# Optimization experiments

Hardware: AMD Instinct MI355X
Metric: run time of the kernel (lower is better)

Reference implementation:

```python
import jax, jax.numpy as jnp
import numpy as np
from jax import lax

B, S, K, D = 256, 256, 64, 128


def setup_inputs() -> dict:
    key = jax.random.key(0)
    k0, k1, k2, k3, k4, k5 = jax.random.split(key, 6)
    encoded_sents = jax.random.normal(k0, (B, S, D), dtype=jnp.float32)
    mask = jax.random.randint(k1, (B, S), 0, 2) > 0  # bool sentence-availability mask
    keys = jax.random.normal(k2, (B, K, D), dtype=jnp.float32) * 0.1
    U = jax.random.normal(k3, (D, D), dtype=jnp.float32) * 0.05
    V = jax.random.normal(k4, (D, D), dtype=jnp.float32) * 0.05
    W = jax.random.normal(k5, (D, D), dtype=jnp.float32) * 0.05
    return {"encoded_sents": encoded_sents, "mask": mask, "keys": keys,
            "U": U, "V": V, "W": W}


def reference(encoded_sents, mask, keys, U, V, W):
    """Recurrent entity network (return_last=True).

    encoded_sents: [B, S, D]; mask: [B, S] bool; keys: [B, K, D]; U/V/W: [D, D].
    Original TF code gathers active batch rows per step, runs EntityCell, and
    scatters the delta back; mathematically equivalent to a masked update over
    the full batch, expressed here as a lax.scan over time.
    """
    def step(h, xm):
        s, m = xm                      # s: [B, D], m: [B] bool
        # gate g_i = sigmoid(s . (h_i + k_i))  -> [B, K]
        g = jax.nn.sigmoid(jnp.einsum('bd,bkd->bk', s, h + keys))
        # h_tilde = act(hU + kV + sW)  -> [B, K, D]
        h_tilde = jax.nn.relu(
            jnp.einsum('bkd,de->bke', h, U)
            + jnp.einsum('bkd,de->bke', keys, V)
            + jnp.einsum('bd,de->be', s, W)[:, None, :]
        )
        upd = h + g[..., None] * h_tilde
        # tf.nn.l2_normalize along last axis
        upd = upd / jnp.sqrt(jnp.maximum(jnp.sum(upd * upd, axis=-1, keepdims=True), 1e-12))
        # scatter-back semantics: only active rows change
        h_new = jnp.where(m[:, None, None], upd, h)
        return h_new, None

    h0 = jnp.zeros_like(keys)  # get_initial_state() tiled over batch
    h_final, _ = lax.scan(step, h0, (encoded_sents.transpose(1, 0, 2), mask.T))
    return h_final  # [B, K, D]
```

## Files before the change

kernel.cpp:

```cpp
#include <hip/hip_runtime.h>
#include <math.h>

#define BB 256
#define SS 256
#define KK 64
#define DD 128

typedef short bf16x8 __attribute__((ext_vector_type(8)));
typedef float f32x4 __attribute__((ext_vector_type(4)));

__device__ __forceinline__ unsigned short bf16_rne(float x) {
  unsigned u = __float_as_uint(x);
  unsigned r = ((u >> 16) & 1u) + 0x7fffu;
  return (unsigned short)((u + r) >> 16);
}

__global__ __launch_bounds__(256) void kv_kernel(const float* __restrict__ keys,
                                                 const float* __restrict__ V,
                                                 float* __restrict__ kV)
{
    __shared__ __align__(16) float Ks[KK][DD];
    __shared__ __align__(16) float Vs[DD][DD];
    const int b = blockIdx.x;
    const int t = threadIdx.x;
    const float* kb = keys + (size_t)b * KK * DD;
    for (int i = t; i < KK * DD / 4; i += 256) ((float4*)Ks)[i] = ((const float4*)kb)[i];
    for (int i = t; i < DD * DD / 4; i += 256) ((float4*)Vs)[i] = ((const float4*)V)[i];
    __syncthreads();

    const int e0 = (t & 15) * 8;
    const int k0 = (t >> 4) * 4;
    float acc[4][8];
#pragma unroll
    for (int i = 0; i < 4; ++i)
#pragma unroll
        for (int j = 0; j < 8; ++j) acc[i][j] = 0.f;

#pragma unroll 4
    for (int d = 0; d < DD; ++d) {
        float aa[4] = {Ks[k0 + 0][d], Ks[k0 + 1][d], Ks[k0 + 2][d], Ks[k0 + 3][d]};
        float4 v0 = *(const float4*)&Vs[d][e0];
        float4 v1 = *(const float4*)&Vs[d][e0 + 4];
        float vv[8] = {v0.x, v0.y, v0.z, v0.w, v1.x, v1.y, v1.z, v1.w};
#pragma unroll
        for (int i = 0; i < 4; ++i)
#pragma unroll
            for (int j = 0; j < 8; ++j) acc[i][j] = fmaf(aa[i], vv[j], acc[i][j]);
    }
    float* o = kV + (size_t)b * KK * DD;
#pragma unroll
    for (int i = 0; i < 4; ++i)
#pragma unroll
        for (int j = 0; j < 8; j += 4) {
            float4 w4 = {acc[i][j], acc[i][j + 1], acc[i][j + 2], acc[i][j + 3]};
            *(float4*)&o[(k0 + i) * DD + e0 + j] = w4;
        }
}

__global__ __launch_bounds__(256) void sw_kernel(const float* __restrict__ enc,
                                                 const float* __restrict__ W,
                                                 float* __restrict__ sW)
{
    __shared__ __align__(16) float Es[64][DD];
    __shared__ __align__(16) float Ws[DD][DD];
    const int blk = blockIdx.x;
    const int b = blk >> 2;
    const int tt = blk & 3;
    const int t = threadIdx.x;
    const float* eb = enc + ((size_t)b * SS + tt * 64) * DD;
    for (int i = t; i < 64 * DD / 4; i += 256) ((float4*)Es)[i] = ((const float4*)eb)[i];
    for (int i = t; i < DD * DD / 4; i += 256) ((float4*)Ws)[i] = ((const float4*)W)[i];
    __syncthreads();

    const int e0 = (t & 15) * 8;
    const int r0 = (t >> 4) * 4;
    float acc[4][8];
#pragma unroll
    for (int i = 0; i < 4; ++i)
#pragma unroll
        for (int j = 0; j < 8; ++j) acc[i][j] = 0.f;

#pragma unroll 4
    for (int d = 0; d < DD; ++d) {
        float aa[4] = {Es[r0 + 0][d], Es[r0 + 1][d], Es[r0 + 2][d], Es[r0 + 3][d]};
        float4 v0 = *(const float4*)&Ws[d][e0];
        float4 v1 = *(const float4*)&Ws[d][e0 + 4];
        float vv[8] = {v0.x, v0.y, v0.z, v0.w, v1.x, v1.y, v1.z, v1.w};
#pragma unroll
        for (int i = 0; i < 4; ++i)
#pragma unroll
            for (int j = 0; j < 8; ++j) acc[i][j] = fmaf(aa[i], vv[j], acc[i][j]);
    }
    float* o = sW + ((size_t)b * SS + tt * 64) * DD;
#pragma unroll
    for (int i = 0; i < 4; ++i)
#pragma unroll
        for (int j = 0; j < 8; j += 4) {
            float4 w4 = {acc[i][j], acc[i][j + 1], acc[i][j + 2], acc[i][j + 3]};
            *(float4*)&o[(r0 + i) * DD + e0 + j] = w4;
        }
}

__global__ __launch_bounds__(256) void sk_kernel(const float* __restrict__ enc,
                                                 const float* __restrict__ keys,
                                                 float* __restrict__ sk)
{
    __shared__ __align__(16) float Es[64][DD];
    __shared__ __align__(16) float Ks[KK][DD];
    const int blk = blockIdx.x;
    const int b = blk >> 2;
    const int tt = blk & 3;
    const int t = threadIdx.x;
    const float* eb = enc + ((size_t)b * SS + tt * 64) * DD;
    const float* kb = keys + (size_t)b * KK * DD;
    for (int i = t; i < 64 * DD / 4; i += 256) ((float4*)Es)[i] = ((const float4*)eb)[i];
    for (int i = t; i < KK * DD / 4; i += 256) ((float4*)Ks)[i] = ((const float4*)kb)[i];
    __syncthreads();

    const int r0 = (t >> 4) * 4;
    const int k0 = (t & 15) * 4;
    float acc[4][4];
#pragma unroll
    for (int i = 0; i < 4; ++i)
#pragma unroll
        for (int j = 0; j < 4; ++j) acc[i][j] = 0.f;

#pragma unroll 4
    for (int d = 0; d < DD; ++d) {
        float er[4], kr[4];
#pragma unroll
        for (int i = 0; i < 4; ++i) er[i] = Es[r0 + i][d];
#pragma unroll
        for (int j = 0; j < 4; ++j) kr[j] = Ks[k0 + j][d];
#pragma unroll
        for (int i = 0; i < 4; ++i)
#pragma unroll
            for (int j = 0; j < 4; ++j) acc[i][j] = fmaf(er[i], kr[j], acc[i][j]);
    }
    float* o = sk + ((size_t)b * SS + tt * 64) * KK;
#pragma unroll
    for (int i = 0; i < 4; ++i) {
        float4 w4 = {acc[i][0], acc[i][1], acc[i][2], acc[i][3]};
        *(float4*)&o[(r0 + i) * KK + k0] = w4;
    }
}

__global__ void ufrag_kernel(const float* __restrict__ U,
                             unsigned short* __restrict__ Ufh,
                             unsigned short* __restrict__ Ufl)
{
    const int blk = blockIdx.x;
    const int ntg = blk >> 2, kt = blk & 3;
    const int l = threadIdx.x;
    const int e = ntg * 16 + (l & 15);
    const int d0 = kt * 32 + (l >> 4) * 8;
#pragma unroll
    for (int j = 0; j < 8; ++j) {
        float x = U[(d0 + j) * DD + e];
        unsigned short hi = bf16_rne(x);
        float rem = x - __uint_as_float(((unsigned)hi) << 16);
        unsigned short lo = bf16_rne(rem);
        int idx = (blk * 64 + l) * 8 + j;
        Ufh[idx] = hi;
        Ufl[idx] = lo;
    }
}

__global__ __launch_bounds__(512, 2) void entnet_main(
    const float* __restrict__ enc,
    const int*   __restrict__ mask,
    const float* __restrict__ sWg,
    const float* __restrict__ skg,
    const float* __restrict__ kVg,
    const unsigned short* __restrict__ Ufh,
    const unsigned short* __restrict__ Ufl,
    float*       __restrict__ out)
{
    __shared__ __align__(16) unsigned short hAhi[4][4][64][8];
    __shared__ __align__(16) unsigned short hAlo[4][4][64][8];
    __shared__ __align__(16) unsigned short shi_sh[2][DD];
    __shared__ __align__(16) unsigned short slo_sh[2][DD];
    __shared__ __align__(16) float sW_sh[2][DD];
    __shared__ __align__(16) float sk_sh[2][KK];
    __shared__ float g_sh[KK];
    __shared__ float rowsq_sh[2][KK];
    __shared__ int act_sh[SS];
    __shared__ int m_sh[SS];
    __shared__ int nact_sh;

    const int b = blockIdx.x;
    const int t = threadIdx.x;
    const int w = t >> 6, l = t & 63;
    const int mt = w & 3, eh = w >> 2;
    const int gi = l >> 4, li = l & 15;
    const int slot_r = l ^ ((l >> 2) & 3);
    const int role = t >> 7;

    if (t < SS) m_sh[t] = mask[b * SS + t];
    {
        unsigned int* p = (unsigned int*)&hAhi[0][0][0][0];
        unsigned int* q = (unsigned int*)&hAlo[0][0][0][0];
        for (int i = t; i < 4 * 4 * 64 * 8 / 2; i += 512) { p[i] = 0u; q[i] = 0u; }
    }
    __syncthreads();
    if (t == 0) {
        int c = 0;
        for (int i = 0; i < SS; ++i) if (m_sh[i]) act_sh[c++] = i;
        nact_sh = c;
    }

    bf16x8 ufh[4][4], ufl[4][4];
#pragma unroll
    for (int nt = 0; nt < 4; ++nt)
#pragma unroll
        for (int kt = 0; kt < 4; ++kt) {
            int ntg = eh * 4 + nt;
            int off = ((ntg * 4 + kt) * 64 + l) * 8;
            ufh[nt][kt] = *(const bf16x8*)&Ufh[off];
            ufl[nt][kt] = *(const bf16x8*)&Ufl[off];
        }
    float kvreg[4][4];
#pragma unroll
    for (int nt = 0; nt < 4; ++nt)
#pragma unroll
        for (int reg = 0; reg < 4; ++reg) {
            int k = 16 * mt + 4 * gi + reg;
            int e = 64 * eh + 16 * nt + li;
            kvreg[nt][reg] = kVg[((size_t)b * KK + k) * DD + e];
        }
    f32x4 hreg[4];
#pragma unroll
    for (int nt = 0; nt < 4; ++nt) hreg[nt] = (f32x4){0.f, 0.f, 0.f, 0.f};
    __syncthreads();

    const int nact = nact_sh;
    if (nact > 0 && t < 320) {
        int t0i = act_sh[0];
        if (role == 0) {
            float x = enc[((size_t)b * SS + t0i) * DD + t];
            unsigned u = __float_as_uint(x);
            shi_sh[0][t] = (unsigned short)(u >> 16);
            float rem = x - __uint_as_float(u & 0xffff0000u);
            slo_sh[0][t] = (unsigned short)(__float_as_uint(rem) >> 16);
        } else if (role == 1) {
            sW_sh[0][t - 128] = sWg[((size_t)b * SS + t0i) * DD + (t - 128)];
        } else {
            sk_sh[0][t - 256] = skg[((size_t)b * SS + t0i) * KK + (t - 256)];
        }
    }
    __syncthreads();

    for (int ai = 0; ai < nact; ++ai) {
        const int cur = ai & 1, nxt = cur ^ 1;
        float pf = 0.f;
        const bool have = (ai + 1 < nact);
        if (have && t < 320) {
            int tn = act_sh[ai + 1];
            if (role == 0)      pf = enc[((size_t)b * SS + tn) * DD + t];
            else if (role == 1) pf = sWg[((size_t)b * SS + tn) * DD + (t - 128)];
            else                pf = skg[((size_t)b * SS + tn) * KK + (t - 256)];
        }

        f32x4 acc[4];
#pragma unroll
        for (int nt = 0; nt < 4; ++nt) acc[nt] = (f32x4){0.f, 0.f, 0.f, 0.f};
        f32x4 gacc = (f32x4){0.f, 0.f, 0.f, 0.f};
#pragma unroll
        for (int kt = 0; kt < 4; ++kt) {
            bf16x8 ah = *(const bf16x8*)&hAhi[kt][mt][slot_r][0];
            bf16x8 al = *(const bf16x8*)&hAlo[kt][mt][slot_r][0];
#pragma unroll
            for (int nt = 0; nt < 4; ++nt) {
                acc[nt] = __builtin_amdgcn_mfma_f32_16x16x32_bf16(ah, ufh[nt][kt], acc[nt], 0, 0, 0);
                acc[nt] = __builtin_amdgcn_mfma_f32_16x16x32_bf16(al, ufh[nt][kt], acc[nt], 0, 0, 0);
                acc[nt] = __builtin_amdgcn_mfma_f32_16x16x32_bf16(ah, ufl[nt][kt], acc[nt], 0, 0, 0);
            }
            if (eh == 0) {
                bf16x8 sh = *(const bf16x8*)&shi_sh[cur][32 * kt + 8 * gi];
                bf16x8 sl = *(const bf16x8*)&slo_sh[cur][32 * kt + 8 * gi];
                gacc = __builtin_amdgcn_mfma_f32_16x16x32_bf16(ah, sh, gacc, 0, 0, 0);
                gacc = __builtin_amdgcn_mfma_f32_16x16x32_bf16(al, sh, gacc, 0, 0, 0);
                gacc = __builtin_amdgcn_mfma_f32_16x16x32_bf16(ah, sl, gacc, 0, 0, 0);
            }
        }
        if (eh == 0 && li == 0) {
#pragma unroll
            for (int reg = 0; reg < 4; ++reg) {
                int k = 16 * mt + 4 * gi + reg;
                float x = gacc[reg] + sk_sh[cur][k];
                g_sh[k] = 1.f / (1.f + __expf(-x));
            }
        }
        __syncthreads();

        float g4[4], sw4[4];
#pragma unroll
        for (int reg = 0; reg < 4; ++reg) g4[reg] = g_sh[16 * mt + 4 * gi + reg];
#pragma unroll
        for (int nt = 0; nt < 4; ++nt) sw4[nt] = sW_sh[cur][64 * eh + 16 * nt + li];
        f32x4 upd[4];
        float ss[4] = {0.f, 0.f, 0.f, 0.f};
#pragma unroll
        for (int nt = 0; nt < 4; ++nt)
#pragma unroll
            for (int reg = 0; reg < 4; ++reg) {
                float v = acc[nt][reg] + kvreg[nt][reg] + sw4[nt];
                v = fmaxf(v, 0.f);
                float u = fmaf(g4[reg], v, hreg[nt][reg]);
                upd[nt][reg] = u;
                ss[reg] = fmaf(u, u, ss[reg]);
            }
#pragma unroll
        for (int m = 1; m < 16; m <<= 1)
#pragma unroll
            for (int reg = 0; reg < 4; ++reg) ss[reg] += __shfl_xor(ss[reg], m);
        if (li == 0) {
#pragma unroll
            for (int reg = 0; reg < 4; ++reg)
                rowsq_sh[eh][16 * mt + 4 * gi + reg] = ss[reg];
        }
        __syncthreads();

        float rinv[4];
#pragma unroll
        for (int reg = 0; reg < 4; ++reg) {
            float tot = ss[reg] + rowsq_sh[1 - eh][16 * mt + 4 * gi + reg];
            rinv[reg] = rsqrtf(fmaxf(tot, 1e-12f));
        }
#pragma unroll
        for (int nt = 0; nt < 4; ++nt) {
            int kt_w = 2 * eh + (nt >> 1);
            int b23  = (2 * nt + (li >> 3)) & 3;
            int j    = l & 7;
#pragma unroll
            for (int reg = 0; reg < 4; ++reg) {
                float hn = upd[nt][reg] * rinv[reg];
                hreg[nt][reg] = hn;
                unsigned u = __float_as_uint(hn);
                unsigned short hi = (unsigned short)(u >> 16);
                float rem = hn - __uint_as_float(u & 0xffff0000u);
                unsigned short lo = (unsigned short)(__float_as_uint(rem) >> 16);
                int le = (4 * gi + reg) | (b23 << 4);
                int slot_w = le ^ ((le >> 2) & 3);
                hAhi[kt_w][mt][slot_w][j] = hi;
                hAlo[kt_w][mt][slot_w][j] = lo;
            }
        }
        if (have && t < 320) {
            if (role == 0) {
                unsigned u = __float_as_uint(pf);
                shi_sh[nxt][t] = (unsigned short)(u >> 16);
                float rem = pf - __uint_as_float(u & 0xffff0000u);
                slo_sh[nxt][t] = (unsigned short)(__float_as_uint(rem) >> 16);
            } else if (role == 1) sW_sh[nxt][t - 128] = pf;
            else                  sk_sh[nxt][t - 256] = pf;
        }
        __syncthreads();
    }

#pragma unroll
    for (int nt = 0; nt < 4; ++nt)
#pragma unroll
        for (int reg = 0; reg < 4; ++reg) {
            int k = 16 * mt + 4 * gi + reg;
            int e = 64 * eh + 16 * nt + li;
            out[((size_t)b * KK + k) * DD + e] = hreg[nt][reg];
        }
}

extern "C" void kernel_launch(void* const* d_in, const int* in_sizes, int n_in,
                              void* d_out, int out_size, void* d_ws, size_t ws_size,
                              hipStream_t stream)
{
    const float* enc  = (const float*)d_in[0];
    const int*   mask = (const int*)  d_in[1];
    const float* keys = (const float*)d_in[2];
    const float* U    = (const float*)d_in[3];
    const float* V    = (const float*)d_in[4];
    const float* W    = (const float*)d_in[5];
    float* out = (float*)d_out;

    float* sW = (float*)d_ws;
    float* sk = sW + (size_t)BB * SS * DD;
    float* kV = sk + (size_t)BB * SS * KK;
    unsigned short* Ufh = (unsigned short*)(kV + (size_t)BB * KK * DD);
    unsigned short* Ufl = Ufh + 8 * 4 * 64 * 8;

    kv_kernel<<<BB, 256, 0, stream>>>(keys, V, kV);
    sw_kernel<<<BB * 4, 256, 0, stream>>>(enc, W, sW);
    sk_kernel<<<BB * 4, 256, 0, stream>>>(enc, keys, sk);
    ufrag_kernel<<<32, 64, 0, stream>>>(U, Ufh, Ufl);
    entnet_main<<<BB, 512, 0, stream>>>(enc, mask, sW, sk, kV, Ufh, Ufl, out);
}
```

Baseline: 494.3 us.

## Split each batch row across four blocks by key rows and fuse sW/sk kernels

The main recurrent kernel is repartitioned so that each batch item's 64 key rows are divided among four 256-thread blocks, each owning 16 rows, instead of one 512-thread block per batch. This launches 1024 blocks rather than 256, which fills more compute units and shortens the per-step serial chain. The gate dot product is now split across the four waves and combined through shared memory. Block indices are remapped so the four blocks of a batch land on the same XCD, and the sW and sk precompute kernels are fused into one launch that reuses the loaded encoder tile. In exchange, every block redundantly loads the s/sW vectors and keeps its own copy of the U fragments.

New measurement: 648.0 us. 1.31x slower.

```diff
diff --git a/kernel.cpp b/kernel.cpp
--- a/kernel.cpp
+++ b/kernel.cpp
@@ -57,9 +57,11 @@
         }
 }
 
-__global__ __launch_bounds__(256) void sw_kernel(const float* __restrict__ enc,
-                                                 const float* __restrict__ W,
-                                                 float* __restrict__ sW)
+__global__ __launch_bounds__(256) void swsk_kernel(const float* __restrict__ enc,
+                                                   const float* __restrict__ W,
+                                                   const float* __restrict__ keys,
+                                                   float* __restrict__ sW,
+                                                   float* __restrict__ sk)
 {
     __shared__ __align__(16) float Es[64][DD];
     __shared__ __align__(16) float Ws[DD][DD];
@@ -72,76 +74,66 @@
     for (int i = t; i < DD * DD / 4; i += 256) ((float4*)Ws)[i] = ((const float4*)W)[i];
     __syncthreads();
 
-    const int e0 = (t & 15) * 8;
-    const int r0 = (t >> 4) * 4;
-    float acc[4][8];
-#pragma unroll
-    for (int i = 0; i < 4; ++i)
-#pragma unroll
-        for (int j = 0; j < 8; ++j) acc[i][j] = 0.f;
-
+    {
+        const int e0 = (t & 15) * 8;
+        const int r0 = (t >> 4) * 4;
+        float acc[4][8];
+#pragma unroll
+        for (int i = 0; i < 4; ++i)
+#pragma unroll
+            for (int j = 0; j < 8; ++j) acc[i][j] = 0.f;
 #pragma unroll 4
-    for (int d = 0; d < DD; ++d) {
-        float aa[4] = {Es[r0 + 0][d], Es[r0 + 1][d], Es[r0 + 2][d], Es[r0 + 3][d]};
-        float4 v0 = *(const float4*)&Ws[d][e0];
-        float4 v1 = *(const float4*)&Ws[d][e0 + 4];
-        float vv[8] = {v0.x, v0.y, v0.z, v0.w, v1.x, v1.y, v1.z, v1.w};
+        for (int d = 0; d < DD; ++d) {
+            float aa[4] = {Es[r0 + 0][d], Es[r0 + 1][d], Es[r0 + 2][d], Es[r0 + 3][d]};
+            float4 v0 = *(const float4*)&Ws[d][e0];
+            float4 v1 = *(const float4*)&Ws[d][e0 + 4];
+            float vv[8] = {v0.x, v0.y, v0.z, v0.w, v1.x, v1.y, v1.z, v1.w};
+#pragma unroll
+            for (int i = 0; i < 4; ++i)
+#pragma unroll
+                for (int j = 0; j < 8; ++j) acc[i][j] = fmaf(aa[i], vv[j], acc[i][j]);
+        }
+        float* o = sW + ((size_t)b * SS + tt * 64) * DD;
 #pragma unroll
         for (int i = 0; i < 4; ++i)
 #pragma unroll
-            for (int j = 0; j < 8; ++j) acc[i][j] = fmaf(aa[i], vv[j], acc[i][j]);
-    }
-    float* o = sW + ((size_t)b * SS + tt * 64) * DD;
-#pragma unroll
-    for (int i = 0; i < 4; ++i)
-#pragma unroll
-        for (int j = 0; j < 8; j += 4) {
-            float4 w4 = {acc[i][j], acc[i][j + 1], acc[i][j + 2], acc[i][j + 3]};
-            *(float4*)&o[(r0 + i) * DD + e0 + j] = w4;
-        }
-}
-
-__global__ __launch_bounds__(256) void sk_kernel(const float* __restrict__ enc,
-                                                 const float* __restrict__ keys,
-                                                 float* __restrict__ sk)
-{
-    __shared__ __align__(16) float Es[64][DD];
-    __shared__ __align__(16) float Ks[KK][DD];
-    const int blk = blockIdx.x;
-    const int b = blk >> 2;
-    const int tt = blk & 3;
-    const int t = threadIdx.x;
-    const float* eb = enc + ((size_t)b * SS + tt * 64) * DD;
-    const float* kb = keys + (size_t)b * KK * DD;
-    for (int i = t; i < 64 * DD / 4; i += 256) ((float4*)Es)[i] = ((const float4*)eb)[i];
-    for (int i = t; i < KK * DD / 4; i += 256) ((float4*)Ks)[i] = ((const float4*)kb)[i];
-    __syncthreads();
-
-    const int r0 = (t >> 4) * 4;
-    const int k0 = (t & 15) * 4;
-    float acc[4][4];
-#pragma unroll
-    for (int i = 0; i < 4; ++i)
-#pragma unroll
-        for (int j = 0; j < 4; ++j) acc[i][j] = 0.f;
-
+            for (int j = 0; j < 8; j += 4) {
+                float4 w4 = {acc[i][j], acc[i][j + 1], acc[i][j + 2], acc[i][j + 3]};
+                *(float4*)&o[(r0 + i) * DD + e0 + j] = w4;
+            }
+    }
+    __syncthreads();
+    {
+        float (*Ks)[DD] = (float(*)[DD])Ws;
+        const float* kb = keys + (size_t)b * KK * DD;
+        for (int i = t; i < KK * DD / 4; i += 256) ((float4*)Ks)[i] = ((const float4*)kb)[i];
+        __syncthreads();
+
+        const int r0 = (t >> 4) * 4;
+        const int k0 = (t & 15) * 4;
+        float acc[4][4];
+#pragma unroll
+        for (int i = 0; i < 4; ++i)
+#pragma unroll
+            for (int j = 0; j < 4; ++j) acc[i][j] = 0.f;
 #pragma unroll 4
-    for (int d = 0; d < DD; ++d) {
-        float er[4], kr[4];
-#pragma unroll
-        for (int i = 0; i < 4; ++i) er[i] = Es[r0 + i][d];
-#pragma unroll
-        for (int j = 0; j < 4; ++j) kr[j] = Ks[k0 + j][d];
-#pragma unroll
-        for (int i = 0; i < 4; ++i)
-#pragma unroll
-            for (int j = 0; j < 4; ++j) acc[i][j] = fmaf(er[i], kr[j], acc[i][j]);
-    }
-    float* o = sk + ((size_t)b * SS + tt * 64) * KK;
-#pragma unroll
-    for (int i = 0; i < 4; ++i) {
-        float4 w4 = {acc[i][0], acc[i][1], acc[i][2], acc[i][3]};
-        *(float4*)&o[(r0 + i) * KK + k0] = w4;
+        for (int d = 0; d < DD; ++d) {
+            float er[4], kr[4];
+#pragma unroll
+            for (int i = 0; i < 4; ++i) er[i] = Es[r0 + i][d];
+#pragma unroll
+            for (int j = 0; j < 4; ++j) kr[j] = Ks[k0 + j][d];
+#pragma unroll
+            for (int i = 0; i < 4; ++i)
+#pragma unroll
+                for (int j = 0; j < 4; ++j) acc[i][j] = fmaf(er[i], kr[j], acc[i][j]);
+        }
+        float* o = sk + ((size_t)b * SS + tt * 64) * KK;
+#pragma unroll
+        for (int i = 0; i < 4; ++i) {
+            float4 w4 = {acc[i][0], acc[i][1], acc[i][2], acc[i][3]};
+            *(float4*)&o[(r0 + i) * KK + k0] = w4;
+        }
     }
 }
 
@@ -150,8 +142,8 @@
                              unsigned short* __restrict__ Ufl)
 {
     const int blk = blockIdx.x;
+    const int l = threadIdx.x;
     const int ntg = blk >> 2, kt = blk & 3;
-    const int l = threadIdx.x;
     const int e = ntg * 16 + (l & 15);
     const int d0 = kt * 32 + (l >> 4) * 8;
 #pragma unroll
@@ -166,7 +158,7 @@
     }
 }
 
-__global__ __launch_bounds__(512, 2) void entnet_main(
+__global__ __launch_bounds__(256, 4) void entnet_main(
     const float* __restrict__ enc,
     const int*   __restrict__ mask,
     const float* __restrict__ sWg,
@@ -176,31 +168,33 @@
     const unsigned short* __restrict__ Ufl,
     float*       __restrict__ out)
 {
-    __shared__ __align__(16) unsigned short hAhi[4][4][64][8];
-    __shared__ __align__(16) unsigned short hAlo[4][4][64][8];
+    __shared__ __align__(16) unsigned short hAhi[4][64][8];
+    __shared__ __align__(16) unsigned short hAlo[4][64][8];
     __shared__ __align__(16) unsigned short shi_sh[2][DD];
     __shared__ __align__(16) unsigned short slo_sh[2][DD];
     __shared__ __align__(16) float sW_sh[2][DD];
-    __shared__ __align__(16) float sk_sh[2][KK];
-    __shared__ float g_sh[KK];
-    __shared__ float rowsq_sh[2][KK];
+    __shared__ __align__(16) float sk_sh[2][16];
+    __shared__ __align__(16) float gpart_sh[4][16];
+    __shared__ __align__(16) float rowsq_sh[4][16];
     __shared__ int act_sh[SS];
     __shared__ int m_sh[SS];
     __shared__ int nact_sh;
 
-    const int b = blockIdx.x;
+    const int raw = blockIdx.x;
+    const int xcd = raw & 7, slot = raw >> 3;
+    const int b = xcd * 32 + (slot >> 2);
+    const int rg = slot & 3;
+
     const int t = threadIdx.x;
     const int w = t >> 6, l = t & 63;
-    const int mt = w & 3, eh = w >> 2;
     const int gi = l >> 4, li = l & 15;
     const int slot_r = l ^ ((l >> 2) & 3);
-    const int role = t >> 7;
 
     if (t < SS) m_sh[t] = mask[b * SS + t];
     {
-        unsigned int* p = (unsigned int*)&hAhi[0][0][0][0];
-        unsigned int* q = (unsigned int*)&hAlo[0][0][0][0];
-        for (int i = t; i < 4 * 4 * 64 * 8 / 2; i += 512) { p[i] = 0u; q[i] = 0u; }
+        unsigned int* p = (unsigned int*)&hAhi[0][0][0];
+        unsigned int* q = (unsigned int*)&hAlo[0][0][0];
+        for (int i = t; i < 4 * 64 * 8 / 2; i += 256) { p[i] = 0u; q[i] = 0u; }
     }
     __syncthreads();
     if (t == 0) {
@@ -209,73 +203,70 @@
         nact_sh = c;
     }
 
-    bf16x8 ufh[4][4], ufl[4][4];
-#pragma unroll
-    for (int nt = 0; nt < 4; ++nt)
+    bf16x8 ufh[2][4], ufl[2][4];
+#pragma unroll
+    for (int nt = 0; nt < 2; ++nt)
 #pragma unroll
         for (int kt = 0; kt < 4; ++kt) {
-            int ntg = eh * 4 + nt;
-            int off = ((ntg * 4 + kt) * 64 + l) * 8;
+            int off = (((2 * w + nt) * 4 + kt) * 64 + l) * 8;
             ufh[nt][kt] = *(const bf16x8*)&Ufh[off];
             ufl[nt][kt] = *(const bf16x8*)&Ufl[off];
         }
-    float kvreg[4][4];
-#pragma unroll
-    for (int nt = 0; nt < 4; ++nt)
+    float kvreg[2][4];
+#pragma unroll
+    for (int nt = 0; nt < 2; ++nt)
 #pragma unroll
         for (int reg = 0; reg < 4; ++reg) {
-            int k = 16 * mt + 4 * gi + reg;
-            int e = 64 * eh + 16 * nt + li;
+            int k = 16 * rg + 4 * gi + reg;
+            int e = 32 * w + 16 * nt + li;
             kvreg[nt][reg] = kVg[((size_t)b * KK + k) * DD + e];
         }
-    f32x4 hreg[4];
-#pragma unroll
-    for (int nt = 0; nt < 4; ++nt) hreg[nt] = (f32x4){0.f, 0.f, 0.f, 0.f};
+    f32x4 hreg[2];
+    hreg[0] = (f32x4){0.f, 0.f, 0.f, 0.f};
+    hreg[1] = (f32x4){0.f, 0.f, 0.f, 0.f};
     __syncthreads();
 
     const int nact = nact_sh;
-    if (nact > 0 && t < 320) {
+    if (nact > 0) {
         int t0i = act_sh[0];
-        if (role == 0) {
+        if (t < 128) {
             float x = enc[((size_t)b * SS + t0i) * DD + t];
             unsigned u = __float_as_uint(x);
             shi_sh[0][t] = (unsigned short)(u >> 16);
             float rem = x - __uint_as_float(u & 0xffff0000u);
             slo_sh[0][t] = (unsigned short)(__float_as_uint(rem) >> 16);
-        } else if (role == 1) {
+        } else {
             sW_sh[0][t - 128] = sWg[((size_t)b * SS + t0i) * DD + (t - 128)];
-        } else {
-            sk_sh[0][t - 256] = skg[((size_t)b * SS + t0i) * KK + (t - 256)];
-        }
+        }
+        if (t < 16) sk_sh[0][t] = skg[((size_t)b * SS + t0i) * KK + 16 * rg + t];
     }
     __syncthreads();
 
     for (int ai = 0; ai < nact; ++ai) {
         const int cur = ai & 1, nxt = cur ^ 1;
-        float pf = 0.f;
+        float pf = 0.f, pfk = 0.f;
         const bool have = (ai + 1 < nact);
-        if (have && t < 320) {
+        if (have) {
             int tn = act_sh[ai + 1];
-            if (role == 0)      pf = enc[((size_t)b * SS + tn) * DD + t];
-            else if (role == 1) pf = sWg[((size_t)b * SS + tn) * DD + (t - 128)];
-            else                pf = skg[((size_t)b * SS + tn) * KK + (t - 256)];
-        }
-
-        f32x4 acc[4];
-#pragma unroll
-        for (int nt = 0; nt < 4; ++nt) acc[nt] = (f32x4){0.f, 0.f, 0.f, 0.f};
+            if (t < 128) pf = enc[((size_t)b * SS + tn) * DD + t];
+            else         pf = sWg[((size_t)b * SS + tn) * DD + (t - 128)];
+            if (t < 16)  pfk = skg[((size_t)b * SS + tn) * KK + 16 * rg + t];
+        }
+
+        f32x4 acc0 = (f32x4){0.f, 0.f, 0.f, 0.f};
+        f32x4 acc1 = (f32x4){0.f, 0.f, 0.f, 0.f};
         f32x4 gacc = (f32x4){0.f, 0.f, 0.f, 0.f};
 #pragma unroll
         for (int kt = 0; kt < 4; ++kt) {
-            bf16x8 ah = *(const bf16x8*)&hAhi[kt][mt][slot_r][0];
-            bf16x8 al = *(const bf16x8*)&hAlo[kt][mt][slot_r][0];
-#pragma unroll
-            for (int nt = 0; nt < 4; ++nt) {
-                acc[nt] = __builtin_amdgcn_mfma_f32_16x16x32_bf16(ah, ufh[nt][kt], acc[nt], 0, 0, 0);
-                acc[nt] = __builtin_amdgcn_mfma_f32_16x16x32_bf16(al, ufh[nt][kt], acc[nt], 0, 0, 0);
-                acc[nt] = __builtin_amdgcn_mfma_f32_16x16x32_bf16(ah, ufl[nt][kt], acc[nt], 0, 0, 0);
-            }
-            if (eh == 0) {
+            bf16x8 ah = *(const bf16x8*)&hAhi[kt][slot_r][0];
+            bf16x8 al = *(const bf16x8*)&hAlo[kt][slot_r][0];
+            acc0 = __builtin_amdgcn_mfma_f32_16x16x32_bf16(ah, ufh[0][kt], acc0, 0, 0, 0);
+            acc0 = __builtin_amdgcn_mfma_f32_16x16x32_bf16(al, ufh[0][kt], acc0, 0, 0, 0);
+            acc0 = __builtin_amdgcn_mfma_f32_16x16x32_bf16(ah, ufl[0][kt], acc0, 0, 0, 0);
+            acc1 = __builtin_amdgcn_mfma_f32_16x16x32_bf16(ah, ufh[1][kt], acc1, 0, 0, 0);
+            acc1 = __builtin_amdgcn_mfma_f32_16x16x32_bf16(al, ufh[1][kt], acc1, 0, 0, 0);
+            acc1 = __builtin_amdgcn_mfma_f32_16x16x32_bf16(ah, ufl[1][kt], acc1, 0, 0, 0);
+            if (w == kt) {
                 bf16x8 sh = *(const bf16x8*)&shi_sh[cur][32 * kt + 8 * gi];
                 bf16x8 sl = *(const bf16x8*)&slo_sh[cur][32 * kt + 8 * gi];
                 gacc = __builtin_amdgcn_mfma_f32_16x16x32_bf16(ah, sh, gacc, 0, 0, 0);
@@ -283,55 +274,55 @@
                 gacc = __builtin_amdgcn_mfma_f32_16x16x32_bf16(ah, sl, gacc, 0, 0, 0);
             }
         }
-        if (eh == 0 && li == 0) {
-#pragma unroll
-            for (int reg = 0; reg < 4; ++reg) {
-                int k = 16 * mt + 4 * gi + reg;
-                float x = gacc[reg] + sk_sh[cur][k];
-                g_sh[k] = 1.f / (1.f + __expf(-x));
-            }
-        }
+        if (li == 0) *(f32x4*)&gpart_sh[w][4 * gi] = gacc;
         __syncthreads();
 
-        float g4[4], sw4[4];
-#pragma unroll
-        for (int reg = 0; reg < 4; ++reg) g4[reg] = g_sh[16 * mt + 4 * gi + reg];
-#pragma unroll
-        for (int nt = 0; nt < 4; ++nt) sw4[nt] = sW_sh[cur][64 * eh + 16 * nt + li];
-        f32x4 upd[4];
+        f32x4 gp = *(const f32x4*)&gpart_sh[0][4 * gi];
+        gp += *(const f32x4*)&gpart_sh[1][4 * gi];
+        gp += *(const f32x4*)&gpart_sh[2][4 * gi];
+        gp += *(const f32x4*)&gpart_sh[3][4 * gi];
+        f32x4 sk4 = *(const f32x4*)&sk_sh[cur][4 * gi];
+        float g4[4];
+#pragma unroll
+        for (int reg = 0; reg < 4; ++reg)
+            g4[reg] = 1.f / (1.f + __expf(-(gp[reg] + sk4[reg])));
+
+        float sw2[2] = { sW_sh[cur][32 * w + li], sW_sh[cur][32 * w + 16 + li] };
+        f32x4 upd[2];
         float ss[4] = {0.f, 0.f, 0.f, 0.f};
 #pragma unroll
-        for (int nt = 0; nt < 4; ++nt)
-#pragma unroll
-            for (int reg = 0; reg < 4; ++reg) {
-                float v = acc[nt][reg] + kvreg[nt][reg] + sw4[nt];
-                v = fmaxf(v, 0.f);
-                float u = fmaf(g4[reg], v, hreg[nt][reg]);
-                upd[nt][reg] = u;
-                ss[reg] = fmaf(u, u, ss[reg]);
-            }
+        for (int reg = 0; reg < 4; ++reg) {
+            float v0 = fmaxf(acc0[reg] + kvreg[0][reg] + sw2[0], 0.f);
+            float u0 = fmaf(g4[reg], v0, hreg[0][reg]);
+            upd[0][reg] = u0;
+            float v1 = fmaxf(acc1[reg] + kvreg[1][reg] + sw2[1], 0.f);
+            float u1 = fmaf(g4[reg], v1, hreg[1][reg]);
+            upd[1][reg] = u1;
+            ss[reg] = fmaf(u0, u0, fmaf(u1, u1, 0.f));
+        }
 #pragma unroll
         for (int m = 1; m < 16; m <<= 1)
 #pragma unroll
             for (int reg = 0; reg < 4; ++reg) ss[reg] += __shfl_xor(ss[reg], m);
         if (li == 0) {
-#pragma unroll
-            for (int reg = 0; reg < 4; ++reg)
-                rowsq_sh[eh][16 * mt + 4 * gi + reg] = ss[reg];
+            f32x4 rr = {ss[0], ss[1], ss[2], ss[3]};
+            *(f32x4*)&rowsq_sh[w][4 * gi] = rr;
         }
         __syncthreads();
 
+        f32x4 rq = *(const f32x4*)&rowsq_sh[0][4 * gi];
+        rq += *(const f32x4*)&rowsq_sh[1][4 * gi];
+        rq += *(const f32x4*)&rowsq_sh[2][4 * gi];
+        rq += *(const f32x4*)&rowsq_sh[3][4 * gi];
         float rinv[4];
 #pragma unroll
-        for (int reg = 0; reg < 4; ++reg) {
-            float tot = ss[reg] + rowsq_sh[1 - eh][16 * mt + 4 * gi + reg];
-            rinv[reg] = rsqrtf(fmaxf(tot, 1e-12f));
-        }
-#pragma unroll
-        for (int nt = 0; nt < 4; ++nt) {
-            int kt_w = 2 * eh + (nt >> 1);
-            int b23  = (2 * nt + (li >> 3)) & 3;
-            int j    = l & 7;
+        for (int reg = 0; reg < 4; ++reg)
+            rinv[reg] = rsqrtf(fmaxf(rq[reg], 1e-12f));
+
+#pragma unroll
+        for (int nt = 0; nt < 2; ++nt) {
+            int b23 = (2 * nt + (li >> 3)) & 3;
+            int j = l & 7;
 #pragma unroll
             for (int reg = 0; reg < 4; ++reg) {
                 float hn = upd[nt][reg] * rinv[reg];
@@ -342,28 +333,30 @@
                 unsigned short lo = (unsigned short)(__float_as_uint(rem) >> 16);
                 int le = (4 * gi + reg) | (b23 << 4);
                 int slot_w = le ^ ((le >> 2) & 3);
-                hAhi[kt_w][mt][slot_w][j] = hi;
-                hAlo[kt_w][mt][slot_w][j] = lo;
+                hAhi[w][slot_w][j] = hi;
+                hAlo[w][slot_w][j] = lo;
             }
         }
-        if (have && t < 320) {
-            if (role == 0) {
+        if (have) {
+            if (t < 128) {
                 unsigned u = __float_as_uint(pf);
                 shi_sh[nxt][t] = (unsigned short)(u >> 16);
                 float rem = pf - __uint_as_float(u & 0xffff0000u);
                 slo_sh[nxt][t] = (unsigned short)(__float_as_uint(rem) >> 16);
-            } else if (role == 1) sW_sh[nxt][t - 128] = pf;
-            else                  sk_sh[nxt][t - 256] = pf;
+            } else {
+                sW_sh[nxt][t - 128] = pf;
+            }
+            if (t < 16) sk_sh[nxt][t] = pfk;
         }
         __syncthreads();
     }
 
 #pragma unroll
-    for (int nt = 0; nt < 4; ++nt)
+    for (int nt = 0; nt < 2; ++nt)
 #pragma unroll
         for (int reg = 0; reg < 4; ++reg) {
-            int k = 16 * mt + 4 * gi + reg;
-            int e = 64 * eh + 16 * nt + li;
+            int k = 16 * rg + 4 * gi + reg;
+            int e = 32 * w + 16 * nt + li;
             out[((size_t)b * KK + k) * DD + e] = hreg[nt][reg];
         }
 }
@@ -387,8 +380,7 @@
     unsigned short* Ufl = Ufh + 8 * 4 * 64 * 8;
 
     kv_kernel<<<BB, 256, 0, stream>>>(keys, V, kV);
-    sw_kernel<<<BB * 4, 256, 0, stream>>>(enc, W, sW);
-    sk_kernel<<<BB * 4, 256, 0, stream>>>(enc, keys, sk);
+    swsk_kernel<<<BB * 4, 256, 0, stream>>>(enc, W, keys, sW, sk);
     ufrag_kernel<<<32, 64, 0, stream>>>(U, Ufh, Ufl);
-    entnet_main<<<BB, 512, 0, stream>>>(enc, mask, sW, sk, kV, Ufh, Ufl, out);
-}
+    entnet_main<<<BB * 4, 256, 0, stream>>>(enc, mask, sW, sk, kV, Ufh, Ufl, out);
+}
```
